# Kernel tuning notes

Measured on AMD Instinct MI355X. Metric: run time of the kernel, lower is better.

## Reference

```python
import jax, jax.numpy as jnp
import numpy as np

B, S, D, H = 2, 2048, 1024, 16
DH = D // H  # key_dim = embed_dim // num_heads
NEG = 1e9    # Keras masked-softmax adder magnitude
EPS = 1e-6


def setup_inputs() -> dict:
    key = jax.random.key(0)
    ks = jax.random.split(key, 6)
    sc = 1.0 / np.sqrt(D)
    return {
        "x": jax.random.normal(ks[0], (B, S, D), jnp.float32),
        "Wq": jax.random.normal(ks[1], (D, H, DH), jnp.float32) * sc,
        "bq": jnp.zeros((H, DH), jnp.float32),
        "Wk": jax.random.normal(ks[2], (D, H, DH), jnp.float32) * sc,
        "bk": jnp.zeros((H, DH), jnp.float32),
        "Wv": jax.random.normal(ks[3], (D, H, DH), jnp.float32) * sc,
        "bv": jnp.zeros((H, DH), jnp.float32),
        "Wo": jax.random.normal(ks[4], (H, DH, D), jnp.float32) * (1.0 / np.sqrt(D)),
        "bo": jnp.zeros((D,), jnp.float32),
        "gamma": jnp.ones((D,), jnp.float32),
        "beta": jnp.zeros((D,), jnp.float32),
    }


def reference(x, Wq, bq, Wk, bk, Wv, bv, Wo, bo, gamma, beta):
    # Keras MultiHeadAttention(query=x, value=x), inference (dropouts are identity)
    q = jnp.einsum("bsd,dhk->bshk", x, Wq) + bq  # [B,S,H,DH]
    k = jnp.einsum("bsd,dhk->bshk", x, Wk) + bk
    v = jnp.einsum("bsd,dhk->bshk", x, Wv) + bv

    scores = jnp.einsum("bqhd,bkhd->bhqk", q, k) / jnp.sqrt(jnp.asarray(DH, x.dtype))
    # Source: mask = 1 - band_part(ones, -1, 0) -> ones strictly ABOVE diagonal.
    # Keras attends where mask==1 and adds (1-mask)*(-1e9) elsewhere. Faithful:
    i = jnp.arange(S)[:, None]
    j = jnp.arange(S)[None, :]
    allowed = (j > i).astype(scores.dtype)  # [S,S], strict upper triangle
    scores = scores + (allowed - 1.0) * NEG  # subtract 1e9 where not allowed
    probs = jax.nn.softmax(scores, axis=-1)

    ctx = jnp.einsum("bhqk,bkhd->bqhd", probs, v)  # [B,S,H,DH]
    attn_out = jnp.einsum("bqhd,hdo->bqo", ctx, Wo) + bo  # [B,S,D]

    # residual + LayerNorm(eps=1e-6)
    y = x + attn_out
    mu = jnp.mean(y, axis=-1, keepdims=True)
    var = jnp.mean(jnp.square(y - mu), axis=-1, keepdims=True)
    return (y - mu) * jax.lax.rsqrt(var + EPS) * gamma + beta
```

## Files before the change

kernel.cpp:

```cpp
#include <hip/hip_runtime.h>
#include <hip/hip_bf16.h>

typedef __hip_bfloat16 bf16;
typedef __attribute__((ext_vector_type(8))) short bf16x8;
typedef __attribute__((ext_vector_type(4))) float f32x4;

constexpr int Bc  = 2;
constexpr int Sc  = 2048;
constexpr int Dc  = 1024;
constexpr int Hc  = 16;
constexpr int DHc = 64;
constexpr int BS  = Bc * Sc;
constexpr int NT  = Sc / 64;

__device__ __forceinline__ float bs2f(unsigned short u) {
    union { unsigned int i; float f; } v; v.i = ((unsigned int)u) << 16; return v.f;
}
__device__ __forceinline__ short f2bs(float x) {
    bf16 h = __float2bfloat16(x);
    return *reinterpret_cast<short*>(&h);
}

typedef const __attribute__((address_space(1))) unsigned int* as1_u32p;
typedef __attribute__((address_space(3))) unsigned int* as3_u32p;
__device__ __forceinline__ void gl_lds16(const void* g, void* l) {
    __builtin_amdgcn_global_load_lds((as1_u32p)g, (as3_u32p)l, 16, 0, 0);
}

__global__ __launch_bounds__(256) void cast_x(const float* __restrict__ in,
                                              short* __restrict__ out) {
    const int i = (blockIdx.x * 256 + threadIdx.x) * 4;
    const float4 v = *(const float4*)(in + i);
    ushort4 o;
    o.x = (unsigned short)f2bs(v.x);
    o.y = (unsigned short)f2bs(v.y);
    o.z = (unsigned short)f2bs(v.z);
    o.w = (unsigned short)f2bs(v.w);
    *(ushort4*)(out + i) = o;
}

__global__ __launch_bounds__(256) void transpose_cast(
    const float* __restrict__ w0, const float* __restrict__ w1,
    const float* __restrict__ w2, const float* __restrict__ w3,
    short* __restrict__ outbase)
{
    __shared__ float T[64][65];
    const int z = blockIdx.z;
    const float* in = (z == 0) ? w0 : (z == 1) ? w1 : (z == 2) ? w2 : w3;
    short* out = outbase + (size_t)z * 1024 * 1024;
    const int k0 = blockIdx.x * 64, n0 = blockIdx.y * 64;
    const int t = threadIdx.x;
    #pragma unroll
    for (int it = 0; it < 4; ++it) {
        const int s = it * 256 + t;
        const int r = s >> 4, c = (s & 15) * 4;
        *(float4*)&T[r][c] = *(const float4*)(in + (size_t)(k0 + r) * 1024 + n0 + c);
    }
    __syncthreads();
    #pragma unroll
    for (int it = 0; it < 4; ++it) {
        const int s = it * 256 + t;
        const int rr = s >> 4, cc = (s & 15) * 4;
        ushort4 o;
        o.x = (unsigned short)f2bs(T[cc + 0][rr]);
        o.y = (unsigned short)f2bs(T[cc + 1][rr]);
        o.z = (unsigned short)f2bs(T[cc + 2][rr]);
        o.w = (unsigned short)f2bs(T[cc + 3][rr]);
        *(ushort4*)(out + (size_t)(n0 + rr) * 1024 + k0 + cc) = o;
    }
}

__global__ __launch_bounds__(256, 3) void gemm_bt(
    const short* __restrict__ A, const short* __restrict__ BTbase,
    const float* __restrict__ b0, const float* __restrict__ b1,
    const float* __restrict__ b2, short* __restrict__ Cbase)
{
    __shared__ __align__(16) short As[128 * 64];
    __shared__ __align__(16) short Bs[128 * 64];

    const int z = blockIdx.z;
    const short* BT = BTbase + (size_t)z * 1024 * 1024;
    const float* bias = (z == 0) ? b0 : (z == 1) ? b1 : b2;
    short* C = Cbase + (size_t)z * BS * Dc;

    const int t = threadIdx.x;
    const int lane = t & 63, w = t >> 6;
    const int quad = lane >> 4, l16 = lane & 15;
    const int wm = (w & 1) * 64, wn = (w >> 1) * 64;
    const int row0 = blockIdx.y * 128;
    const int col0 = blockIdx.x * 128;
    const int sw = l16 & 7;

    f32x4 acc[4][4] = {};

    for (int kt = 0; kt < 1024; kt += 64) {
        __syncthreads();
        #pragma unroll
        for (int i = 0; i < 4; ++i) {
            const int f = i * 256 + t;
            const int r = f >> 3;
            const int g = (f & 7) ^ (r & 7);
            short* lb = &As[(i * 256 + w * 64) * 8];
            gl_lds16(A + (size_t)(row0 + r) * 1024 + kt + g * 8, lb);
            short* lb2 = &Bs[(i * 256 + w * 64) * 8];
            gl_lds16(BT + (size_t)(col0 + r) * 1024 + kt + g * 8, lb2);
        }
        __syncthreads();
        #pragma unroll
        for (int ks = 0; ks < 2; ++ks) {
            bf16x8 av[4], bv[4];
            #pragma unroll
            for (int mt = 0; mt < 4; ++mt) {
                const int r = wm + mt * 16 + l16;
                av[mt] = *(const bf16x8*)&As[r * 64 + ((ks * 4 + quad) ^ sw) * 8];
            }
            #pragma unroll
            for (int nt = 0; nt < 4; ++nt) {
                const int r = wn + nt * 16 + l16;
                bv[nt] = *(const bf16x8*)&Bs[r * 64 + ((ks * 4 + quad) ^ sw) * 8];
            }
            #pragma unroll
            for (int mt = 0; mt < 4; ++mt)
                #pragma unroll
                for (int nt = 0; nt < 4; ++nt)
                    acc[mt][nt] = __builtin_amdgcn_mfma_f32_16x16x32_bf16(
                        av[mt], bv[nt], acc[mt][nt], 0, 0, 0);
        }
    }

    float bvv[4];
    #pragma unroll
    for (int nt = 0; nt < 4; ++nt) bvv[nt] = bias[col0 + wn + nt * 16 + l16];
    #pragma unroll
    for (int mt = 0; mt < 4; ++mt)
        #pragma unroll
        for (int reg = 0; reg < 4; ++reg) {
            const size_t row = row0 + wm + mt * 16 + quad * 4 + reg;
            #pragma unroll
            for (int nt = 0; nt < 4; ++nt) {
                const int col = col0 + wn + nt * 16 + l16;
                C[row * 1024 + col] = f2bs(acc[mt][nt][reg] + bvv[nt]);
            }
        }
}


template<bool DIAG>
__device__ __forceinline__ void qtile_step(
    const bf16x8 (&qf)[2],
    const short (&Ks)[64][72], const short (&VsT)[64][72],
    short (&Psw)[16][72],
    const int k0, const int row_base,
    const int quad, const int l16,
    float (&l)[4], f32x4 (&O)[4])
{
    bf16x8 kf[2][4];
    #pragma unroll
    for (int ks = 0; ks < 2; ++ks)
        #pragma unroll
        for (int nt = 0; nt < 4; ++nt)
            kf[ks][nt] = *(const bf16x8*)&Ks[nt * 16 + l16][ks * 32 + quad * 8];

    f32x4 S[4] = {};
    #pragma unroll
    for (int ks = 0; ks < 2; ++ks)
        #pragma unroll
        for (int nt = 0; nt < 4; ++nt)
            S[nt] = __builtin_amdgcn_mfma_f32_16x16x32_bf16(qf[ks], kf[ks][nt], S[nt], 0, 0, 0);

    #pragma unroll
    for (int nt = 0; nt < 4; ++nt) {
        #pragma unroll
        for (int reg = 0; reg < 4; ++reg) {
            float s = fminf(S[nt][reg] * 0.18033688f, 115.4f);
            if (DIAG) {
                const int col = k0 + nt * 16 + l16;
                const int row = row_base + quad * 4 + reg;
                s = (col > row) ? s : -126.0f;
            }
            const float p = exp2f(s);
            S[nt][reg] = p;
            l[reg] += p;
        }
    }

    #pragma unroll
    for (int reg = 0; reg < 4; ++reg) {
        const __hip_bfloat162 lo = __float22bfloat162_rn(make_float2(S[0][reg], S[1][reg]));
        const __hip_bfloat162 hi = __float22bfloat162_rn(make_float2(S[2][reg], S[3][reg]));
        uint2 u;
        u.x = *reinterpret_cast<const unsigned int*>(&lo);
        u.y = *reinterpret_cast<const unsigned int*>(&hi);
        *(uint2*)&Psw[quad * 4 + reg][l16 * 4] = u;
    }

    #pragma unroll
    for (int ks = 0; ks < 2; ++ks) {
        const bf16x8 pf = *(const bf16x8*)&Psw[l16][ks * 32 + quad * 8];
        #pragma unroll
        for (int nt = 0; nt < 4; ++nt) {
            const bf16x8 vf = *(const bf16x8*)&VsT[nt * 16 + l16][ks * 32 + quad * 8];
            O[nt] = __builtin_amdgcn_mfma_f32_16x16x32_bf16(pf, vf, O[nt], 0, 0, 0);
        }
    }
}

__global__ __launch_bounds__(256, 3) void attn_mfma(
    const short* __restrict__ Qg, const short* __restrict__ Kg,
    const short* __restrict__ Vg, short* __restrict__ CTX)
{
    __shared__ __align__(16) short Ks [2][64][72];
    __shared__ __align__(16) short VsT[2][64][72];
    __shared__ __align__(16) short Ps[4][16][72];

    const int tid  = threadIdx.x;
    const int lane = tid & 63, w = tid >> 6;
    const int quad = lane >> 4, l16 = lane & 15;

    const int f  = blockIdx.x + 32 * blockIdx.y + 512 * blockIdx.z;
    const int r_ = (f & 7) * 128 + (f >> 3);
    const int xq = r_ & 31;
    const int h  = (r_ >> 5) & 15;
    const int b  = r_ >> 9;
    const size_t rb = (size_t)b * Sc;
    const int cb = h * DHc;

    const int myq = (xq & 1) ? (NT - 1 - (xq >> 1)) : (xq >> 1);
    const int t0  = myq;
    const int q0  = myq * 64;

    bf16x8 qf[2];
    {
        const short* qp = Qg + (rb + q0 + w * 16 + l16) * (size_t)Dc + cb + quad * 8;
        qf[0] = *(const bf16x8*)(qp);
        qf[1] = *(const bf16x8*)(qp + 32);
    }
    float l[4] = {};
    f32x4 O[4] = {};

    const int skey = tid & 63, sseg = (tid >> 6) * 8;
    const int pkey = ((skey & 15) << 2) | (skey >> 4);

    {
        const int buf = t0 & 1;
        const size_t g = (rb + t0 * 64 + skey) * (size_t)Dc + cb + sseg;
        const bf16x8 k0v = *(const bf16x8*)(Kg + g);
        const bf16x8 k1v = *(const bf16x8*)(Kg + g + 32);
        const bf16x8 v0v = *(const bf16x8*)(Vg + g);
        const bf16x8 v1v = *(const bf16x8*)(Vg + g + 32);
        *(bf16x8*)&Ks[buf][skey][sseg]      = k0v;
        *(bf16x8*)&Ks[buf][skey][sseg + 32] = k1v;
        #pragma unroll
        for (int e = 0; e < 8; ++e) {
            VsT[buf][sseg + e][pkey]      = v0v[e];
            VsT[buf][sseg + 32 + e][pkey] = v1v[e];
        }
    }
    __syncthreads();

    for (int t = t0; t < NT; ++t) {
        const int cur = t & 1;
        const bool havenext = (t + 1 < NT);
        bf16x8 pk0, pk1, pv0, pv1;
        if (havenext) {
            const size_t g = (rb + (t + 1) * 64 + skey) * (size_t)Dc + cb + sseg;
            pk0 = *(const bf16x8*)(Kg + g);
            pk1 = *(const bf16x8*)(Kg + g + 32);
            pv0 = *(const bf16x8*)(Vg + g);
            pv1 = *(const bf16x8*)(Vg + g + 32);
        }

        if (t == t0)
            qtile_step<true >(qf, Ks[cur], VsT[cur], Ps[w],
                              t * 64, q0 + w * 16, quad, l16, l, O);
        else
            qtile_step<false>(qf, Ks[cur], VsT[cur], Ps[w],
                              t * 64, q0 + w * 16, quad, l16, l, O);

        if (havenext) {
            const int nb = cur ^ 1;
            *(bf16x8*)&Ks[nb][skey][sseg]      = pk0;
            *(bf16x8*)&Ks[nb][skey][sseg + 32] = pk1;
            #pragma unroll
            for (int e = 0; e < 8; ++e) {
                VsT[nb][sseg + e][pkey]      = pv0[e];
                VsT[nb][sseg + 32 + e][pkey] = pv1[e];
            }
            __syncthreads();
        }
    }

    #pragma unroll
    for (int off = 1; off < 16; off <<= 1)
        #pragma unroll
        for (int reg = 0; reg < 4; ++reg)
            l[reg] += __shfl_xor(l[reg], off, 64);
    #pragma unroll
    for (int reg = 0; reg < 4; ++reg) l[reg] = 1.0f / l[reg];
    #pragma unroll
    for (int nt = 0; nt < 4; ++nt)
        #pragma unroll
        for (int reg = 0; reg < 4; ++reg) {
            const size_t row = rb + q0 + w * 16 + quad * 4 + reg;
            CTX[row * Dc + cb + nt * 16 + l16] = f2bs(O[nt][reg] * l[reg]);
        }
}

__global__ __launch_bounds__(256) void vmean(const short* __restrict__ V,
                                             short* __restrict__ CTX)
{
    const int h = blockIdx.x, b = blockIdx.y;
    const int t = threadIdx.x;
    const int dh = t & 63, ck = t >> 6;
    float s = 0.f;
    const short* vp = V + ((size_t)b * Sc + ck * 512) * Dc + h * DHc + dh;
    for (int j = 0; j < 512; ++j) s += bs2f(vp[(size_t)j * Dc]);
    __shared__ float red[4][64];
    red[ck][dh] = s;
    __syncthreads();
    if (ck == 0) {
        const float tot = (red[0][dh] + red[1][dh] + red[2][dh] + red[3][dh]) * (1.f / Sc);
        CTX[((size_t)b * Sc + Sc - 1) * Dc + h * DHc + dh] = f2bs(tot);
    }
}

__global__ __launch_bounds__(256, 4) void resid_ln(
    const float* __restrict__ X, const short* __restrict__ AO,
    const float* __restrict__ gamma, const float* __restrict__ beta,
    float* __restrict__ out)
{
    const int r = blockIdx.x;
    const int t = threadIdx.x;
    const size_t base = (size_t)r * Dc + t * 4;

    const float4 x4 = *(const float4*)(X + base);
    const ushort4 a4 = *(const ushort4*)(AO + base);
    float y[4];
    y[0] = x4.x + bs2f(a4.x);
    y[1] = x4.y + bs2f(a4.y);
    y[2] = x4.z + bs2f(a4.z);
    y[3] = x4.w + bs2f(a4.w);

    float s  = y[0] + y[1] + y[2] + y[3];
    float s2 = y[0]*y[0] + y[1]*y[1] + y[2]*y[2] + y[3]*y[3];
    #pragma unroll
    for (int off = 1; off < 64; off <<= 1) {
        s  += __shfl_xor(s,  off, 64);
        s2 += __shfl_xor(s2, off, 64);
    }
    __shared__ float red[8];
    const int w = t >> 6;
    if ((t & 63) == 0) { red[w] = s; red[4 + w] = s2; }
    __syncthreads();
    s  = red[0] + red[1] + red[2] + red[3];
    s2 = red[4] + red[5] + red[6] + red[7];

    const float mu   = s * (1.0f / Dc);
    const float rstd = rsqrtf(s2 * (1.0f / Dc) - mu * mu + 1e-6f);

    const float4 g4 = *(const float4*)(gamma + t * 4);
    const float4 b4 = *(const float4*)(beta  + t * 4);
    float4 o;
    o.x = (y[0] - mu) * rstd * g4.x + b4.x;
    o.y = (y[1] - mu) * rstd * g4.y + b4.y;
    o.z = (y[2] - mu) * rstd * g4.z + b4.z;
    o.w = (y[3] - mu) * rstd * g4.w + b4.w;
    *(float4*)(out + base) = o;
}

extern "C" void kernel_launch(void* const* d_in, const int* in_sizes, int n_in,
                              void* d_out, int out_size, void* d_ws, size_t ws_size,
                              hipStream_t stream)
{
    (void)in_sizes; (void)n_in; (void)out_size; (void)ws_size;
    const float* x     = (const float*)d_in[0];
    const float* Wq    = (const float*)d_in[1];
    const float* bq    = (const float*)d_in[2];
    const float* Wk    = (const float*)d_in[3];
    const float* bk    = (const float*)d_in[4];
    const float* Wv    = (const float*)d_in[5];
    const float* bv    = (const float*)d_in[6];
    const float* Wo    = (const float*)d_in[7];
    const float* bo    = (const float*)d_in[8];
    const float* gamma = (const float*)d_in[9];
    const float* beta  = (const float*)d_in[10];
    float* out = (float*)d_out;

    const size_t matN = (size_t)BS * Dc;
    const size_t wN   = (size_t)Dc * Dc;
    short* xb = (short*)d_ws;
    short* WT = xb + matN;
    short* Qb = WT + 4 * wN;
    short* Kb = Qb + matN;
    short* Vb = Kb + matN;
    short* Cx = Vb + matN;
    short* AO = Qb;

    cast_x<<<matN / 1024, 256, 0, stream>>>(x, xb);

    dim3 gt(16, 16, 4);
    transpose_cast<<<gt, 256, 0, stream>>>(Wq, Wk, Wv, Wo, WT);

    dim3 gq(Dc / 128, BS / 128, 3);
    gemm_bt<<<gq, 256, 0, stream>>>(xb, WT, bq, bk, bv, Qb);

    dim3 ga(32, Hc, Bc);
    attn_mfma<<<ga, 256, 0, stream>>>(Qb, Kb, Vb, Cx);

    dim3 gv(Hc, Bc);
    vmean<<<gv, 256, 0, stream>>>(Vb, Cx);

    dim3 go(Dc / 128, BS / 128, 1);
    gemm_bt<<<go, 256, 0, stream>>>(Cx, WT + 3 * wN, bo, bo, bo, AO);

    resid_ln<<<BS, 256, 0, stream>>>(x, AO, gamma, beta, out);
}
```

Before: 238.9 us.

## Fold softmax scale into Q GEMM, single-buffer KV, add MFMA priority and remap blocks

The softmax scale and log2e factor now multiply Q in the projection GEMM epilogue, which removes a multiply per score in the attention kernel. K/V shared memory drops from double to single buffering with an extra barrier, and launch bounds rise to 4 blocks per CU to raise occupancy. s_setprio wraps the MFMA sections to favour matrix issue, and the block-to-(b,h,q) mapping is changed so each XCD handles whole heads, aiming for better L2 reuse of K/V. The extra barrier per tile may stall warps, and rounding the scaled Q to bf16 slightly changes numerics.

```diff
diff --git a/kernel.cpp b/kernel.cpp
--- a/kernel.cpp
+++ b/kernel.cpp
@@ -73,7 +73,8 @@
 __global__ __launch_bounds__(256, 3) void gemm_bt(
     const short* __restrict__ A, const short* __restrict__ BTbase,
     const float* __restrict__ b0, const float* __restrict__ b1,
-    const float* __restrict__ b2, short* __restrict__ Cbase)
+    const float* __restrict__ b2, short* __restrict__ Cbase,
+    const float sc0)
 {
     __shared__ __align__(16) short As[128 * 64];
     __shared__ __align__(16) short Bs[128 * 64];
@@ -81,6 +82,7 @@
     const int z = blockIdx.z;
     const short* BT = BTbase + (size_t)z * 1024 * 1024;
     const float* bias = (z == 0) ? b0 : (z == 1) ? b1 : b2;
+    const float sc = (z == 0) ? sc0 : 1.0f;
     short* C = Cbase + (size_t)z * BS * Dc;
 
     const int t = threadIdx.x;
@@ -139,7 +141,7 @@
             #pragma unroll
             for (int nt = 0; nt < 4; ++nt) {
                 const int col = col0 + wn + nt * 16 + l16;
-                C[row * 1024 + col] = f2bs(acc[mt][nt][reg] + bvv[nt]);
+                C[row * 1024 + col] = f2bs((acc[mt][nt][reg] + bvv[nt]) * sc);
             }
         }
 }
@@ -162,17 +164,19 @@
             kf[ks][nt] = *(const bf16x8*)&Ks[nt * 16 + l16][ks * 32 + quad * 8];
 
     f32x4 S[4] = {};
+    __builtin_amdgcn_s_setprio(1);
     #pragma unroll
     for (int ks = 0; ks < 2; ++ks)
         #pragma unroll
         for (int nt = 0; nt < 4; ++nt)
             S[nt] = __builtin_amdgcn_mfma_f32_16x16x32_bf16(qf[ks], kf[ks][nt], S[nt], 0, 0, 0);
+    __builtin_amdgcn_s_setprio(0);
 
     #pragma unroll
     for (int nt = 0; nt < 4; ++nt) {
         #pragma unroll
         for (int reg = 0; reg < 4; ++reg) {
-            float s = fminf(S[nt][reg] * 0.18033688f, 115.4f);
+            float s = fminf(S[nt][reg], 115.4f);
             if (DIAG) {
                 const int col = k0 + nt * 16 + l16;
                 const int row = row_base + quad * 4 + reg;
@@ -194,6 +198,7 @@
         *(uint2*)&Psw[quad * 4 + reg][l16 * 4] = u;
     }
 
+    __builtin_amdgcn_s_setprio(1);
     #pragma unroll
     for (int ks = 0; ks < 2; ++ks) {
         const bf16x8 pf = *(const bf16x8*)&Psw[l16][ks * 32 + quad * 8];
@@ -203,31 +208,35 @@
             O[nt] = __builtin_amdgcn_mfma_f32_16x16x32_bf16(pf, vf, O[nt], 0, 0, 0);
         }
     }
-}
-
-__global__ __launch_bounds__(256, 3) void attn_mfma(
+    __builtin_amdgcn_s_setprio(0);
+}
+
+__global__ __launch_bounds__(256, 4) void attn_mfma(
     const short* __restrict__ Qg, const short* __restrict__ Kg,
     const short* __restrict__ Vg, short* __restrict__ CTX)
 {
-    __shared__ __align__(16) short Ks [2][64][72];
-    __shared__ __align__(16) short VsT[2][64][72];
+    __shared__ __align__(16) short Ks [64][72];
+    __shared__ __align__(16) short VsT[64][72];
     __shared__ __align__(16) short Ps[4][16][72];
 
     const int tid  = threadIdx.x;
     const int lane = tid & 63, w = tid >> 6;
     const int quad = lane >> 4, l16 = lane & 15;
 
-    const int f  = blockIdx.x + 32 * blockIdx.y + 512 * blockIdx.z;
-    const int r_ = (f & 7) * 128 + (f >> 3);
-    const int xq = r_ & 31;
-    const int h  = (r_ >> 5) & 15;
-    const int b  = r_ >> 9;
+    const int f   = blockIdx.x + 32 * blockIdx.y + 512 * blockIdx.z;
+    const int xcd = f & 7;
+    const int loc = f >> 3;
+    const int j   = loc >> 5;
+    const int lq  = loc & 31;
+    const int myq = (j & 1) ? (NT - 1 - lq) : lq;
+    const int bh  = xcd * 4 + j;
+    const int h   = bh & 15;
+    const int b   = bh >> 4;
     const size_t rb = (size_t)b * Sc;
     const int cb = h * DHc;
 
-    const int myq = (xq & 1) ? (NT - 1 - (xq >> 1)) : (xq >> 1);
-    const int t0  = myq;
-    const int q0  = myq * 64;
+    const int t0 = myq;
+    const int q0 = myq * 64;
 
     bf16x8 qf[2];
     {
@@ -242,24 +251,22 @@
     const int pkey = ((skey & 15) << 2) | (skey >> 4);
 
     {
-        const int buf = t0 & 1;
         const size_t g = (rb + t0 * 64 + skey) * (size_t)Dc + cb + sseg;
         const bf16x8 k0v = *(const bf16x8*)(Kg + g);
         const bf16x8 k1v = *(const bf16x8*)(Kg + g + 32);
         const bf16x8 v0v = *(const bf16x8*)(Vg + g);
         const bf16x8 v1v = *(const bf16x8*)(Vg + g + 32);
-        *(bf16x8*)&Ks[buf][skey][sseg]      = k0v;
-        *(bf16x8*)&Ks[buf][skey][sseg + 32] = k1v;
+        *(bf16x8*)&Ks[skey][sseg]      = k0v;
+        *(bf16x8*)&Ks[skey][sseg + 32] = k1v;
         #pragma unroll
         for (int e = 0; e < 8; ++e) {
-            VsT[buf][sseg + e][pkey]      = v0v[e];
-            VsT[buf][sseg + 32 + e][pkey] = v1v[e];
+            VsT[sseg + e][pkey]      = v0v[e];
+            VsT[sseg + 32 + e][pkey] = v1v[e];
         }
     }
     __syncthreads();
 
     for (int t = t0; t < NT; ++t) {
-        const int cur = t & 1;
         const bool havenext = (t + 1 < NT);
         bf16x8 pk0, pk1, pv0, pv1;
         if (havenext) {
@@ -271,20 +278,20 @@
         }
 
         if (t == t0)
-            qtile_step<true >(qf, Ks[cur], VsT[cur], Ps[w],
+            qtile_step<true >(qf, Ks, VsT, Ps[w],
                               t * 64, q0 + w * 16, quad, l16, l, O);
         else
-            qtile_step<false>(qf, Ks[cur], VsT[cur], Ps[w],
+            qtile_step<false>(qf, Ks, VsT, Ps[w],
                               t * 64, q0 + w * 16, quad, l16, l, O);
 
         if (havenext) {
-            const int nb = cur ^ 1;
-            *(bf16x8*)&Ks[nb][skey][sseg]      = pk0;
-            *(bf16x8*)&Ks[nb][skey][sseg + 32] = pk1;
+            __syncthreads();
+            *(bf16x8*)&Ks[skey][sseg]      = pk0;
+            *(bf16x8*)&Ks[skey][sseg + 32] = pk1;
             #pragma unroll
             for (int e = 0; e < 8; ++e) {
-                VsT[nb][sseg + e][pkey]      = pv0[e];
-                VsT[nb][sseg + 32 + e][pkey] = pv1[e];
+                VsT[sseg + e][pkey]      = pv0[e];
+                VsT[sseg + 32 + e][pkey] = pv1[e];
             }
             __syncthreads();
         }
@@ -402,16 +409,16 @@
     transpose_cast<<<gt, 256, 0, stream>>>(Wq, Wk, Wv, Wo, WT);
 
     dim3 gq(Dc / 128, BS / 128, 3);
-    gemm_bt<<<gq, 256, 0, stream>>>(xb, WT, bq, bk, bv, Qb);
-
-    dim3 ga(32, Hc, Bc);
+    gemm_bt<<<gq, 256, 0, stream>>>(xb, WT, bq, bk, bv, Qb, 0.18033688f);
+
+    dim3 ga(32, 16, 2);
     attn_mfma<<<ga, 256, 0, stream>>>(Qb, Kb, Vb, Cx);
 
     dim3 gv(Hc, Bc);
     vmean<<<gv, 256, 0, stream>>>(Vb, Cx);
 
     dim3 go(Dc / 128, BS / 128, 1);
-    gemm_bt<<<go, 256, 0, stream>>>(Cx, WT + 3 * wN, bo, bo, bo, AO);
+    gemm_bt<<<go, 256, 0, stream>>>(Cx, WT + 3 * wN, bo, bo, bo, AO, 1.0f);
 
     resid_ln<<<BS, 256, 0, stream>>>(x, AO, gamma, beta, out);
 }
```

Result: faster. 218.9 us (-8.3%).
